# Kernel optimization log

Hardware: AMD Instinct MI355X
Metric: run time of the kernel (lower is better)

The kernel has to match this reference:

```python
import jax, jax.numpy as jnp
import numpy as np

N_NODES = 100000
N_EDGES = 1600000
N_GRAPHS = 64


def _sage(x, src, dst, Wl, bl, Wr):
    # SAGEConv (mean aggr): out = lin_l(mean_j x_j) + lin_r(x_i)
    msg = x[src]                                             # [E, F] gather
    s = jax.ops.segment_sum(msg, dst, num_segments=N_NODES)  # [N, F]
    cnt = jax.ops.segment_sum(jnp.ones((msg.shape[0],), x.dtype), dst,
                              num_segments=N_NODES)[:, None]
    mean = jnp.where(cnt > 0, s / jnp.maximum(cnt, 1.0), 0.0)
    return mean @ Wl + bl + x @ Wr


def setup_inputs() -> dict:
    key = jax.random.key(0)
    ks = jax.random.split(key, 12)
    sc = lambda f: 1.0 / np.sqrt(f)
    inp = {
        'x':   jax.random.normal(ks[0], (N_NODES, 32), jnp.float32),
        'Wl0': jax.random.normal(ks[1], (32, 64), jnp.float32) * sc(32),
        'bl0': jnp.zeros((64,), jnp.float32),
        'Wr0': jax.random.normal(ks[2], (32, 64), jnp.float32) * sc(32),
        'Wl1': jax.random.normal(ks[3], (64, 64), jnp.float32) * sc(64),
        'bl1': jnp.zeros((64,), jnp.float32),
        'Wr1': jax.random.normal(ks[4], (64, 64), jnp.float32) * sc(64),
        'Wl2': jax.random.normal(ks[5], (64, 64), jnp.float32) * sc(64),
        'bl2': jnp.zeros((64,), jnp.float32),
        'Wr2': jax.random.normal(ks[6], (64, 64), jnp.float32) * sc(64),
        'W_out': jax.random.normal(ks[7], (64, 8), jnp.float32) * sc(64),
        'b_out': jnp.zeros((8,), jnp.float32),
        'edge_index': jax.random.randint(ks[8], (2, N_EDGES), 0, N_NODES, jnp.int32),
        'batch': jnp.sort(jax.random.randint(ks[9], (N_NODES,), 0, N_GRAPHS, jnp.int32)),
    }
    return inp


def reference(x, Wl0, bl0, Wr0, Wl1, bl1, Wr1, Wl2, bl2, Wr2,
              W_out, b_out, edge_index, batch):
    src, dst = edge_index[0], edge_index[1]
    h = _sage(x, src, dst, Wl0, bl0, Wr0)
    h = _sage(h, src, dst, Wl1, bl1, Wr1)
    h = _sage(h, src, dst, Wl2, bl2, Wr2)
    pooled = jax.ops.segment_max(h, batch, num_segments=N_GRAPHS)  # [G, 64]
    logits = pooled @ W_out + b_out
    return jax.nn.log_softmax(logits, axis=-1)
```

## Files before the change

### kernel.cpp

```cpp
#include <hip/hip_runtime.h>
#include <math.h>
#include <stdint.h>

#define N_NODES 100000
#define N_EDGES 1600000
#define N_GRAPHS 64

#define BSH 9
#define NBKT 196
#define NCHUNK 256
#define EPC 6250
#define FLAT (NBKT * NCHUNK)


typedef __attribute__((ext_vector_type(8))) short bf16x8;
typedef __attribute__((ext_vector_type(8))) unsigned short u16x8;
typedef __attribute__((ext_vector_type(4))) float f32x4;

__device__ __forceinline__ void atomicMaxFloat(float* addr, float val) {
    if (val >= 0.0f) {
        atomicMax((int*)addr, __float_as_int(val));
    } else {
        atomicMin((unsigned int*)addr, __float_as_uint(val));
    }
}

__device__ __forceinline__ unsigned short f2bf(float f) {
    unsigned u = __float_as_uint(f);
    unsigned r = (u + 0x7FFFu + ((u >> 16) & 1u)) >> 16;
    return (unsigned short)r;
}
__device__ __forceinline__ float bf2f(unsigned short b) {
    return __uint_as_float(((unsigned)b) << 16);
}

__global__ void k_init(float* __restrict__ pooled) {
    int i = blockIdx.x * blockDim.x + threadIdx.x;
    if (i < N_GRAPHS * 64) pooled[i] = -INFINITY;
}

__global__ __launch_bounds__(256) void k_rhist(const int* __restrict__ dst,
                                               int* __restrict__ S) {
    __shared__ int h[NBKT];
    for (int i = threadIdx.x; i < NBKT; i += 256) h[i] = 0;
    __syncthreads();
    int c = blockIdx.x;
    int e0 = c * EPC;
    for (int e = e0 + threadIdx.x; e < e0 + EPC; e += 256)
        atomicAdd(&h[dst[e] >> BSH], 1);
    __syncthreads();
    for (int i = threadIdx.x; i < NBKT; i += 256) S[i * NCHUNK + c] = h[i];
}

__global__ __launch_bounds__(1024) void k_rscan(int* __restrict__ S) {
    __shared__ int part[1024];
    int t = threadIdx.x;
    const int seg = (FLAT + 1023) / 1024;
    int lo = t * seg;
    int hi = lo + seg; if (hi > FLAT) hi = FLAT;
    int s = 0;
    for (int i = lo; i < hi; ++i) s += S[i];
    part[t] = s;
    __syncthreads();
    for (int off = 1; off < 1024; off <<= 1) {
        int add = (t >= off) ? part[t - off] : 0;
        __syncthreads();
        part[t] += add;
        __syncthreads();
    }
    int ex = (t > 0) ? part[t - 1] : 0;
    if (t == 1023) S[FLAT] = part[1023];
    int run = ex;
    for (int i = lo; i < hi; ++i) { int v = S[i]; S[i] = run; run += v; }
}

__global__ __launch_bounds__(256) void k_rscatter(
    const int* __restrict__ src, const int* __restrict__ dst,
    const int* __restrict__ S, int2* __restrict__ pairs) {
    __shared__ int ofs[NBKT];
    __shared__ int cnt[NBKT];
    int c = blockIdx.x;
    for (int i = threadIdx.x; i < NBKT; i += 256) {
        ofs[i] = S[i * NCHUNK + c];
        cnt[i] = 0;
    }
    __syncthreads();
    int e0 = c * EPC;
    for (int e = e0 + threadIdx.x; e < e0 + EPC; e += 256) {
        int d = dst[e];
        int b = d >> BSH;
        int r = atomicAdd(&cnt[b], 1);
        pairs[ofs[b] + r] = make_int2(src[e], d);
    }
}

__global__ __launch_bounds__(256) void k_rbuild(
    const int2* __restrict__ pairs, const int* __restrict__ S,
    int* __restrict__ row_ptr, int* __restrict__ col) {
    __shared__ int ncnt[512];
    __shared__ int nofs[512];
    __shared__ int part[256];
    int b = blockIdx.x;
    int t = threadIdx.x;
    int base = S[b * NCHUNK];
    int next = (b == NBKT - 1) ? S[FLAT] : S[(b + 1) * NCHUNK];
    int count = next - base;
    int nodeBase = b << BSH;

    ncnt[2 * t] = 0; ncnt[2 * t + 1] = 0;
    __syncthreads();
    for (int i = t; i < count; i += 256)
        atomicAdd(&ncnt[pairs[base + i].y - nodeBase], 1);
    __syncthreads();
    int v0 = ncnt[2 * t], v1 = ncnt[2 * t + 1];
    part[t] = v0 + v1;
    __syncthreads();
    for (int off = 1; off < 256; off <<= 1) {
        int add = (t >= off) ? part[t - off] : 0;
        __syncthreads();
        part[t] += add;
        __syncthreads();
    }
    int ex = (t > 0) ? part[t - 1] : 0;
    nofs[2 * t] = ex;
    nofs[2 * t + 1] = ex + v0;
    ncnt[2 * t] = 0; ncnt[2 * t + 1] = 0;
    __syncthreads();
    for (int i = t; i < 512; i += 256) {
        int node = nodeBase + i;
        if (node < N_NODES) row_ptr[node] = base + nofs[i];
    }
    if (b == 0 && t == 0) row_ptr[N_NODES] = N_EDGES;
    for (int i = t; i < count; i += 256) {
        int2 p = pairs[base + i];
        int li = p.y - nodeBase;
        int r = atomicAdd(&ncnt[li], 1);
        col[base + nofs[li] + r] = p.x;
    }
}

__global__ void k_xcast(const float* __restrict__ x, unsigned short* __restrict__ xhi) {
    int i = blockIdx.x * blockDim.x + threadIdx.x;
    int base = i * 8;
    if (base >= N_NODES * 32) return;
    const float4* xp = (const float4*)(x + base);
    float4 a = xp[0], b = xp[1];
    u16x8 o;
    o[0] = f2bf(a.x); o[1] = f2bf(a.y); o[2] = f2bf(a.z); o[3] = f2bf(a.w);
    o[4] = f2bf(b.x); o[5] = f2bf(b.y); o[6] = f2bf(b.z); o[7] = f2bf(b.w);
    *(u16x8*)(xhi + base) = o;
}

#define NC 8

template <int FIN>
__global__ __launch_bounds__(256) void k_agg_bf(
    const unsigned short* __restrict__ hb,
    const int* __restrict__ row_ptr, const int* __restrict__ col,
    float* __restrict__ mean) {
    int lane = threadIdx.x & 63;
    int wave = blockIdx.x * 4 + (threadIdx.x >> 6);
    int base = wave * NC;
    if (base >= N_NODES) return;
    int rp = row_ptr[base + (lane < NC ? lane : NC)];

    constexpr int G = (FIN == 64) ? 4 : 8;
    constexpr int LPR = 64 / G;
    int g  = lane / LPR;
    int fq = lane % LPR;

    for (int i = 0; i < NC; ++i) {
        int node = base + i;
        int start = __shfl(rp, i);
        int end   = __shfl(rp, i + 1);
        float s0 = 0.0f, s1 = 0.0f, s2 = 0.0f, s3 = 0.0f;

        for (int eb = start; eb < end; eb += 64) {
            int n = end - eb; if (n > 64) n = 64;
            int c = (eb + lane < end) ? col[eb + lane] : 0;
            int j = 0;
            for (; j + 4 * G - 1 < n; j += 4 * G) {
                int cA = __shfl(c, j + g);
                int cB = __shfl(c, j + G + g);
                int cC = __shfl(c, j + 2 * G + g);
                int cD = __shfl(c, j + 3 * G + g);
                ushort4 vA = *(const ushort4*)(hb + (size_t)cA * FIN + fq * 4);
                ushort4 vB = *(const ushort4*)(hb + (size_t)cB * FIN + fq * 4);
                ushort4 vC = *(const ushort4*)(hb + (size_t)cC * FIN + fq * 4);
                ushort4 vD = *(const ushort4*)(hb + (size_t)cD * FIN + fq * 4);
                s0 += (bf2f(vA.x) + bf2f(vB.x)) + (bf2f(vC.x) + bf2f(vD.x));
                s1 += (bf2f(vA.y) + bf2f(vB.y)) + (bf2f(vC.y) + bf2f(vD.y));
                s2 += (bf2f(vA.z) + bf2f(vB.z)) + (bf2f(vC.z) + bf2f(vD.z));
                s3 += (bf2f(vA.w) + bf2f(vB.w)) + (bf2f(vC.w) + bf2f(vD.w));
            }
            for (; j + 2 * G - 1 < n; j += 2 * G) {
                int cA = __shfl(c, j + g);
                int cB = __shfl(c, j + G + g);
                ushort4 vA = *(const ushort4*)(hb + (size_t)cA * FIN + fq * 4);
                ushort4 vB = *(const ushort4*)(hb + (size_t)cB * FIN + fq * 4);
                s0 += bf2f(vA.x) + bf2f(vB.x);
                s1 += bf2f(vA.y) + bf2f(vB.y);
                s2 += bf2f(vA.z) + bf2f(vB.z);
                s3 += bf2f(vA.w) + bf2f(vB.w);
            }
            for (; j + G - 1 < n; j += G) {
                int cA = __shfl(c, j + g);
                ushort4 vA = *(const ushort4*)(hb + (size_t)cA * FIN + fq * 4);
                s0 += bf2f(vA.x);
                s1 += bf2f(vA.y);
                s2 += bf2f(vA.z);
                s3 += bf2f(vA.w);
            }
            if (j < n) {
                int idx = j + g;
                bool valid = idx < n;
                int cA = __shfl(c, valid ? idx : 0);
                ushort4 vA = *(const ushort4*)(hb + (size_t)cA * FIN + fq * 4);
                if (valid) {
                    s0 += bf2f(vA.x);
                    s1 += bf2f(vA.y);
                    s2 += bf2f(vA.z);
                    s3 += bf2f(vA.w);
                }
            }
        }
#pragma unroll
        for (int m = LPR; m < 64; m <<= 1) {
            s0 += __shfl_xor(s0, m);
            s1 += __shfl_xor(s1, m);
            s2 += __shfl_xor(s2, m);
            s3 += __shfl_xor(s3, m);
        }
        int deg = end - start;
        float inv = (deg > 0) ? 1.0f / (float)deg : 0.0f;
        if (lane < LPR) {
            *(float4*)(mean + (size_t)node * 64 + fq * 4) =
                make_float4(s0 * inv, s1 * inv, s2 * inv, s3 * inv);
        }
    }
}

template <int KM, bool XBF, int KX, int XS, bool OUTBF>
__global__ __launch_bounds__(256) void k_dense_mfma(
    const float* mean,
    const float* x,
    const unsigned short* xhi, const unsigned short* xlo,
    const float* __restrict__ Wl, const float* __restrict__ bl,
    const float* __restrict__ Wr,
    float* outf, unsigned short* ohi, unsigned short* olo) {
    int lane = threadIdx.x & 63;
    int strip = blockIdx.x * 4 + (threadIdx.x >> 6);
    if (strip * 16 >= N_NODES) return;
    int row0 = strip * 16;
    int m = lane & 15;
    int g = lane >> 4;

    f32x4 acc[4] = {};

#pragma unroll
    for (int kt = 0; kt < KM / 32; ++kt) {
        int k0 = kt * 32 + g * 8;
        const float4* ap = (const float4*)(mean + (size_t)(row0 + m) * 64 + k0);
        float4 a0 = ap[0], a1 = ap[1];
        float av[8] = {a0.x, a0.y, a0.z, a0.w, a1.x, a1.y, a1.z, a1.w};
        bf16x8 ahi, alo;
#pragma unroll
        for (int j = 0; j < 8; ++j) {
            unsigned short hb = f2bf(av[j]);
            ahi[j] = (short)hb;
            alo[j] = (short)f2bf(av[j] - bf2f(hb));
        }
#pragma unroll
        for (int nt = 0; nt < 4; ++nt) {
            bf16x8 b;
#pragma unroll
            for (int j = 0; j < 8; ++j)
                b[j] = (short)f2bf(Wl[(size_t)(k0 + j) * 64 + nt * 16 + m]);
            acc[nt] = __builtin_amdgcn_mfma_f32_16x16x32_bf16(ahi, b, acc[nt], 0, 0, 0);
            acc[nt] = __builtin_amdgcn_mfma_f32_16x16x32_bf16(alo, b, acc[nt], 0, 0, 0);
        }
    }
#pragma unroll
    for (int kt = 0; kt < KX / 32; ++kt) {
        int k0 = kt * 32 + g * 8;
        bf16x8 ahi, alo;
        if constexpr (XBF) {
            ahi = *(const bf16x8*)(xhi + (size_t)(row0 + m) * XS + k0);
            alo = *(const bf16x8*)(xlo + (size_t)(row0 + m) * XS + k0);
        } else {
            const float4* ap = (const float4*)(x + (size_t)(row0 + m) * XS + k0);
            float4 a0 = ap[0], a1 = ap[1];
            float av[8] = {a0.x, a0.y, a0.z, a0.w, a1.x, a1.y, a1.z, a1.w};
#pragma unroll
            for (int j = 0; j < 8; ++j) {
                unsigned short hb = f2bf(av[j]);
                ahi[j] = (short)hb;
                alo[j] = (short)f2bf(av[j] - bf2f(hb));
            }
        }
#pragma unroll
        for (int nt = 0; nt < 4; ++nt) {
            bf16x8 b;
#pragma unroll
            for (int j = 0; j < 8; ++j)
                b[j] = (short)f2bf(Wr[(size_t)(k0 + j) * 64 + nt * 16 + m]);
            acc[nt] = __builtin_amdgcn_mfma_f32_16x16x32_bf16(ahi, b, acc[nt], 0, 0, 0);
            acc[nt] = __builtin_amdgcn_mfma_f32_16x16x32_bf16(alo, b, acc[nt], 0, 0, 0);
        }
    }
#pragma unroll
    for (int nt = 0; nt < 4; ++nt) {
        float bias = bl[nt * 16 + m];
#pragma unroll
        for (int r = 0; r < 4; ++r) {
            int row = row0 + g * 4 + r;
            float v = acc[nt][r] + bias;
            if constexpr (OUTBF) {
                unsigned short hb = f2bf(v);
                ohi[(size_t)row * 64 + nt * 16 + m] = hb;
                olo[(size_t)row * 64 + nt * 16 + m] = f2bf(v - bf2f(hb));
            } else {
                outf[(size_t)row * 64 + nt * 16 + m] = v;
            }
        }
    }
}

__global__ void k_gbound(const int* __restrict__ batch, int* __restrict__ gstart) {
    int i = blockIdx.x * blockDim.x + threadIdx.x;
    if (i >= N_NODES) return;
    int b = batch[i];
    if (i == 0) {
        for (int g = 0; g <= b; ++g) gstart[g] = 0;
    } else {
        int pb = batch[i - 1];
        for (int g = pb + 1; g <= b; ++g) gstart[g] = i;
    }
    if (i == N_NODES - 1) {
        for (int g = b + 1; g <= N_GRAPHS; ++g) gstart[g] = N_NODES;
    }
}

#define PSPLIT 8
__global__ __launch_bounds__(256) void k_pool2(const float* __restrict__ h,
                                               const int* __restrict__ gstart,
                                               float* __restrict__ pooled) {
    __shared__ float red[4][64];
    int gr = blockIdx.x & 63;
    int split = blockIdx.x >> 6;
    int lane = threadIdx.x & 63;
    int w = threadIdx.x >> 6;
    int s = gstart[gr], e = gstart[gr + 1];
    float m = -INFINITY;
    for (int i = s + split * 4 + w; i < e; i += PSPLIT * 4)
        m = fmaxf(m, h[(size_t)i * 64 + lane]);
    red[w][lane] = m;
    __syncthreads();
    if (w == 0) {
        m = fmaxf(fmaxf(red[0][lane], red[1][lane]),
                  fmaxf(red[2][lane], red[3][lane]));
        if (m > -INFINITY) atomicMaxFloat(&pooled[gr * 64 + lane], m);
    }
}

__global__ void k_head(const float* __restrict__ pooled,
                       const float* __restrict__ Wout,
                       const float* __restrict__ bout, float* __restrict__ out) {
    int tid = threadIdx.x;
    int g = tid >> 3, o = tid & 7;
    float acc = bout[o];
#pragma unroll
    for (int k = 0; k < 64; ++k) acc += pooled[g * 64 + k] * Wout[k * 8 + o];
    float mx = acc;
#pragma unroll
    for (int m = 1; m < 8; m <<= 1) mx = fmaxf(mx, __shfl_xor(mx, m));
    float ex = expf(acc - mx);
    float sum = ex;
#pragma unroll
    for (int m = 1; m < 8; m <<= 1) sum += __shfl_xor(sum, m);
    out[g * 8 + o] = (acc - mx) - logf(sum);
}

extern "C" void kernel_launch(void* const* d_in, const int* in_sizes, int n_in,
                              void* d_out, int out_size, void* d_ws, size_t ws_size,
                              hipStream_t stream) {
    const float* x    = (const float*)d_in[0];
    const float* Wl0  = (const float*)d_in[1];
    const float* bl0  = (const float*)d_in[2];
    const float* Wr0  = (const float*)d_in[3];
    const float* Wl1  = (const float*)d_in[4];
    const float* bl1  = (const float*)d_in[5];
    const float* Wr1  = (const float*)d_in[6];
    const float* Wl2  = (const float*)d_in[7];
    const float* bl2  = (const float*)d_in[8];
    const float* Wr2  = (const float*)d_in[9];
    const float* Wout = (const float*)d_in[10];
    const float* bout = (const float*)d_in[11];
    const int*   eidx = (const int*)d_in[12];
    const int*   batch= (const int*)d_in[13];
    const int* src = eidx;
    const int* dst = eidx + N_EDGES;

    uint8_t* ws = (uint8_t*)d_ws;
    int*   S       = (int*)(ws + 0);
    int*   row_ptr = (int*)(ws + 400128);
    int*   col     = (int*)(ws + 800256);
    float* pooled  = (float*)(ws + 7200384);
    int*   gstart  = (int*)(ws + 7216768);
    float* M       = (float*)(ws + 7217408);
    int2*  pairs   = (int2*)(ws + 7217408);
    unsigned short* Hhi = (unsigned short*)(ws + 32817408);
    unsigned short* Hlo = (unsigned short*)(ws + 45617408);

    k_init<<<16, 256, 0, stream>>>(pooled);
    k_rhist<<<NCHUNK, 256, 0, stream>>>(dst, S);
    k_rscan<<<1, 1024, 0, stream>>>(S);
    k_rscatter<<<NCHUNK, 256, 0, stream>>>(src, dst, S, pairs);
    k_rbuild<<<NBKT, 256, 0, stream>>>(pairs, S, row_ptr, col);
    k_xcast<<<(N_NODES * 32 / 8 + 255) / 256, 256, 0, stream>>>(x, Hhi);
    k_gbound<<<(N_NODES + 255) / 256, 256, 0, stream>>>(batch, gstart);

    int aggBlocks = (N_NODES / NC + 3) / 4;
    int mfmaBlocks = (N_NODES / 16 + 3) / 4;

    k_agg_bf<32><<<aggBlocks, 256, 0, stream>>>(Hhi, row_ptr, col, M);
    k_dense_mfma<32, false, 32, 32, true><<<mfmaBlocks, 256, 0, stream>>>(
        M, x, nullptr, nullptr, Wl0, bl0, Wr0, nullptr, Hhi, Hlo);
    k_agg_bf<64><<<aggBlocks, 256, 0, stream>>>(Hhi, row_ptr, col, M);
    k_dense_mfma<64, true, 64, 64, true><<<mfmaBlocks, 256, 0, stream>>>(
        M, nullptr, Hhi, Hlo, Wl1, bl1, Wr1, nullptr, Hhi, Hlo);
    k_agg_bf<64><<<aggBlocks, 256, 0, stream>>>(Hhi, row_ptr, col, M);
    k_dense_mfma<64, true, 64, 64, false><<<mfmaBlocks, 256, 0, stream>>>(
        M, nullptr, Hhi, Hlo, Wl2, bl2, Wr2, M, nullptr, nullptr);

    k_pool2<<<64 * PSPLIT, 256, 0, stream>>>(M, gstart, pooled);
    k_head<<<1, 512, 0, stream>>>(pooled, Wout, bout, (float*)d_out);
}
```

Before: 254.3 us.

## Pack edge pairs into 32-bit words, fuse prep kernels, store final layer as bf16

```diff
diff --git a/kernel.cpp b/kernel.cpp
--- a/kernel.cpp
+++ b/kernel.cpp
@@ -34,9 +34,33 @@
     return __uint_as_float(((unsigned)b) << 16);
 }
 
-__global__ void k_init(float* __restrict__ pooled) {
+__global__ __launch_bounds__(256) void k_prep(
+    const float* __restrict__ x, unsigned short* __restrict__ xhi,
+    const int* __restrict__ batch, int* __restrict__ gstart,
+    float* __restrict__ pooled) {
     int i = blockIdx.x * blockDim.x + threadIdx.x;
+    if (i < N_NODES * 32 / 8) {
+        int base = i * 8;
+        const float4* xp = (const float4*)(x + base);
+        float4 a = xp[0], b = xp[1];
+        u16x8 o;
+        o[0] = f2bf(a.x); o[1] = f2bf(a.y); o[2] = f2bf(a.z); o[3] = f2bf(a.w);
+        o[4] = f2bf(b.x); o[5] = f2bf(b.y); o[6] = f2bf(b.z); o[7] = f2bf(b.w);
+        *(u16x8*)(xhi + base) = o;
+    }
     if (i < N_GRAPHS * 64) pooled[i] = -INFINITY;
+    if (i < N_NODES) {
+        int b = batch[i];
+        if (i == 0) {
+            for (int g = 0; g <= b; ++g) gstart[g] = 0;
+        } else {
+            int pb = batch[i - 1];
+            for (int g = pb + 1; g <= b; ++g) gstart[g] = i;
+        }
+        if (i == N_NODES - 1) {
+            for (int g = b + 1; g <= N_GRAPHS; ++g) gstart[g] = N_NODES;
+        }
+    }
 }
 
 __global__ __launch_bounds__(256) void k_rhist(const int* __restrict__ dst,
@@ -76,7 +100,7 @@
 
 __global__ __launch_bounds__(256) void k_rscatter(
     const int* __restrict__ src, const int* __restrict__ dst,
-    const int* __restrict__ S, int2* __restrict__ pairs) {
+    const int* __restrict__ S, unsigned int* __restrict__ pairs) {
     __shared__ int ofs[NBKT];
     __shared__ int cnt[NBKT];
     int c = blockIdx.x;
@@ -90,12 +114,12 @@
         int d = dst[e];
         int b = d >> BSH;
         int r = atomicAdd(&cnt[b], 1);
-        pairs[ofs[b] + r] = make_int2(src[e], d);
+        pairs[ofs[b] + r] = ((unsigned)(d & 511) << 17) | (unsigned)src[e];
     }
 }
 
 __global__ __launch_bounds__(256) void k_rbuild(
-    const int2* __restrict__ pairs, const int* __restrict__ S,
+    const unsigned int* __restrict__ pairs, const int* __restrict__ S,
     int* __restrict__ row_ptr, int* __restrict__ col) {
     __shared__ int ncnt[512];
     __shared__ int nofs[512];
@@ -110,7 +134,7 @@
     ncnt[2 * t] = 0; ncnt[2 * t + 1] = 0;
     __syncthreads();
     for (int i = t; i < count; i += 256)
-        atomicAdd(&ncnt[pairs[base + i].y - nodeBase], 1);
+        atomicAdd(&ncnt[pairs[base + i] >> 17], 1);
     __syncthreads();
     int v0 = ncnt[2 * t], v1 = ncnt[2 * t + 1];
     part[t] = v0 + v1;
@@ -132,23 +156,11 @@
     }
     if (b == 0 && t == 0) row_ptr[N_NODES] = N_EDGES;
     for (int i = t; i < count; i += 256) {
-        int2 p = pairs[base + i];
-        int li = p.y - nodeBase;
+        unsigned p = pairs[base + i];
+        int li = p >> 17;
         int r = atomicAdd(&ncnt[li], 1);
-        col[base + nofs[li] + r] = p.x;
-    }
-}
-
-__global__ void k_xcast(const float* __restrict__ x, unsigned short* __restrict__ xhi) {
-    int i = blockIdx.x * blockDim.x + threadIdx.x;
-    int base = i * 8;
-    if (base >= N_NODES * 32) return;
-    const float4* xp = (const float4*)(x + base);
-    float4 a = xp[0], b = xp[1];
-    u16x8 o;
-    o[0] = f2bf(a.x); o[1] = f2bf(a.y); o[2] = f2bf(a.z); o[3] = f2bf(a.w);
-    o[4] = f2bf(b.x); o[5] = f2bf(b.y); o[6] = f2bf(b.z); o[7] = f2bf(b.w);
-    *(u16x8*)(xhi + base) = o;
+        col[base + nofs[li] + r] = (int)(p & 0x1FFFFu);
+    }
 }
 
 #define NC 8
@@ -240,7 +252,7 @@
     }
 }
 
-template <int KM, bool XBF, int KX, int XS, bool OUTBF>
+template <int KM, bool XBF, int KX, int XS, int OM>
 __global__ __launch_bounds__(256) void k_dense_mfma(
     const float* mean,
     const float* x,
@@ -315,10 +327,12 @@
         for (int r = 0; r < 4; ++r) {
             int row = row0 + g * 4 + r;
             float v = acc[nt][r] + bias;
-            if constexpr (OUTBF) {
+            if constexpr (OM == 1) {
                 unsigned short hb = f2bf(v);
                 ohi[(size_t)row * 64 + nt * 16 + m] = hb;
                 olo[(size_t)row * 64 + nt * 16 + m] = f2bf(v - bf2f(hb));
+            } else if constexpr (OM == 2) {
+                ohi[(size_t)row * 64 + nt * 16 + m] = f2bf(v);
             } else {
                 outf[(size_t)row * 64 + nt * 16 + m] = v;
             }
@@ -326,23 +340,8 @@
     }
 }
 
-__global__ void k_gbound(const int* __restrict__ batch, int* __restrict__ gstart) {
-    int i = blockIdx.x * blockDim.x + threadIdx.x;
-    if (i >= N_NODES) return;
-    int b = batch[i];
-    if (i == 0) {
-        for (int g = 0; g <= b; ++g) gstart[g] = 0;
-    } else {
-        int pb = batch[i - 1];
-        for (int g = pb + 1; g <= b; ++g) gstart[g] = i;
-    }
-    if (i == N_NODES - 1) {
-        for (int g = b + 1; g <= N_GRAPHS; ++g) gstart[g] = N_NODES;
-    }
-}
-
 #define PSPLIT 8
-__global__ __launch_bounds__(256) void k_pool2(const float* __restrict__ h,
+__global__ __launch_bounds__(256) void k_pool2(const unsigned short* __restrict__ h,
                                                const int* __restrict__ gstart,
                                                float* __restrict__ pooled) {
     __shared__ float red[4][64];
@@ -353,7 +352,7 @@
     int s = gstart[gr], e = gstart[gr + 1];
     float m = -INFINITY;
     for (int i = s + split * 4 + w; i < e; i += PSPLIT * 4)
-        m = fmaxf(m, h[(size_t)i * 64 + lane]);
+        m = fmaxf(m, bf2f(h[(size_t)i * 64 + lane]));
     red[w][lane] = m;
     __syncthreads();
     if (w == 0) {
@@ -408,31 +407,30 @@
     float* pooled  = (float*)(ws + 7200384);
     int*   gstart  = (int*)(ws + 7216768);
     float* M       = (float*)(ws + 7217408);
-    int2*  pairs   = (int2*)(ws + 7217408);
+    unsigned int* pairs = (unsigned int*)(ws + 7217408);
     unsigned short* Hhi = (unsigned short*)(ws + 32817408);
     unsigned short* Hlo = (unsigned short*)(ws + 45617408);
 
-    k_init<<<16, 256, 0, stream>>>(pooled);
+    k_prep<<<(N_NODES * 32 / 8 + 255) / 256, 256, 0, stream>>>(
+        x, Hhi, batch, gstart, pooled);
     k_rhist<<<NCHUNK, 256, 0, stream>>>(dst, S);
     k_rscan<<<1, 1024, 0, stream>>>(S);
     k_rscatter<<<NCHUNK, 256, 0, stream>>>(src, dst, S, pairs);
     k_rbuild<<<NBKT, 256, 0, stream>>>(pairs, S, row_ptr, col);
-    k_xcast<<<(N_NODES * 32 / 8 + 255) / 256, 256, 0, stream>>>(x, Hhi);
-    k_gbound<<<(N_NODES + 255) / 256, 256, 0, stream>>>(batch, gstart);
 
     int aggBlocks = (N_NODES / NC + 3) / 4;
     int mfmaBlocks = (N_NODES / 16 + 3) / 4;
 
     k_agg_bf<32><<<aggBlocks, 256, 0, stream>>>(Hhi, row_ptr, col, M);
-    k_dense_mfma<32, false, 32, 32, true><<<mfmaBlocks, 256, 0, stream>>>(
+    k_dense_mfma<32, false, 32, 32, 1><<<mfmaBlocks, 256, 0, stream>>>(
         M, x, nullptr, nullptr, Wl0, bl0, Wr0, nullptr, Hhi, Hlo);
     k_agg_bf<64><<<aggBlocks, 256, 0, stream>>>(Hhi, row_ptr, col, M);
-    k_dense_mfma<64, true, 64, 64, true><<<mfmaBlocks, 256, 0, stream>>>(
+    k_dense_mfma<64, true, 64, 64, 1><<<mfmaBlocks, 256, 0, stream>>>(
         M, nullptr, Hhi, Hlo, Wl1, bl1, Wr1, nullptr, Hhi, Hlo);
     k_agg_bf<64><<<aggBlocks, 256, 0, stream>>>(Hhi, row_ptr, col, M);
-    k_dense_mfma<64, true, 64, 64, false><<<mfmaBlocks, 256, 0, stream>>>(
-        M, nullptr, Hhi, Hlo, Wl2, bl2, Wr2, M, nullptr, nullptr);
-
-    k_pool2<<<64 * PSPLIT, 256, 0, stream>>>(M, gstart, pooled);
+    k_dense_mfma<64, true, 64, 64, 2><<<mfmaBlocks, 256, 0, stream>>>(
+        M, nullptr, Hhi, Hlo, Wl2, bl2, Wr2, nullptr, Hhi, nullptr);
+
+    k_pool2<<<64 * PSPLIT, 256, 0, stream>>>(Hhi, gstart, pooled);
     k_head<<<1, 512, 0, stream>>>(pooled, Wout, bout, (float*)d_out);
 }
```

New measurement: 247.6 us. -2.6%, faster.
